# Kernel tuning notes

Hardware: AMD Instinct MI355X
Metric: run time of the kernel (lower is better)

Reference implementation:

```python
import jax, jax.numpy as jnp
import numpy as np

B, S_IN, T_OUT, H, L, V = 64, 512, 64, 1024, 2, 1024


def setup_inputs() -> dict:
    key = jax.random.key(0)
    ks = iter(jax.random.split(key, 64))
    def p(shape, scale=0.02):
        return (jax.random.normal(next(ks), shape, jnp.float32) * scale)
    d = {"x": jax.random.normal(next(ks), (B, 2, S_IN), jnp.float32)}
    d["emb"] = p((V, H))
    for l in range(L):
        i = 2 if l == 0 else H
        d[f"enc_Wih{l}"] = p((3 * H, i)); d[f"enc_Whh{l}"] = p((3 * H, H))
        d[f"enc_bih{l}"] = p((3 * H,));   d[f"enc_bhh{l}"] = p((3 * H,))
        d[f"dec_Wih{l}"] = p((H, H));     d[f"dec_Whh{l}"] = p((H, H))
        d[f"dec_bih{l}"] = p((H,));       d[f"dec_bhh{l}"] = p((H,))
    d["hq_W"] = p((H, H)); d["hq_b"] = p((H,))
    d["comb_W"] = p((H, 2 * H)); d["comb_b"] = p((H,))
    d["fc_W"] = p((V, H)); d["fc_b"] = p((V,))
    return d


def _gru_layer(x_seq, Wih, Whh, bih, bhh):
    # x_seq: [B,T,I] -> (outputs [B,T,H], h_T [B,H]). PyTorch GRU gate order r,z,n.
    xp = jnp.einsum('bti,gi->btg', x_seq, Wih) + bih  # [B,T,3H]
    h0 = jnp.zeros((x_seq.shape[0], Whh.shape[1]), x_seq.dtype)
    def step(h, xpt):
        hp = h @ Whh.T + bhh
        xr, xz, xn = jnp.split(xpt, 3, axis=-1)
        hr, hz, hn = jnp.split(hp, 3, axis=-1)
        r = jax.nn.sigmoid(xr + hr)
        z = jax.nn.sigmoid(xz + hz)
        n = jnp.tanh(xn + r * hn)
        h = (1.0 - z) * n + z * h
        return h, h
    hT, ys = jax.lax.scan(step, h0, jnp.swapaxes(xp, 0, 1))
    return jnp.swapaxes(ys, 0, 1), hT


def _forward(x, emb,
             enc_Wih0, enc_Whh0, enc_bih0, enc_bhh0,
             enc_Wih1, enc_Whh1, enc_bih1, enc_bhh1,
             dec_Wih0, dec_Whh0, dec_bih0, dec_bhh0,
             dec_Wih1, dec_Whh1, dec_bih1, dec_bhh1,
             hq_W, hq_b, comb_W, comb_b, fc_W, fc_b):
    enc_params = [(enc_Wih0, enc_Whh0, enc_bih0, enc_bhh0),
                  (enc_Wih1, enc_Whh1, enc_bih1, enc_bhh1)]
    dec_params = [(dec_Wih0, dec_Whh0, dec_bih0, dec_bhh0),
                  (dec_Wih1, dec_Whh1, dec_bih1, dec_bhh1)]
    # ---- encoder: GRU over x permuted to [B, S_in, 2] ----
    seq = jnp.transpose(x, (0, 2, 1)).astype(jnp.float32)
    h_enc = []
    for (Wih, Whh, bih, bhh) in enc_params:
        seq, hT = _gru_layer(seq, Wih, Whh, bih, bhh)
        h_enc.append(hT)
    enc_outs = seq                      # [B, S_in, H]
    hidden0 = jnp.stack(h_enc, axis=0)  # [L, B, H]

    tok0 = jnp.zeros((B,), jnp.int32)
    def dec_step(carry, _):
        tok, hid = carry
        inp = emb[tok]                  # [B, H]
        new_h = []
        for l, (Wih, Whh, bih, bhh) in enumerate(dec_params):
            h = jnp.tanh(inp @ Wih.T + bih + hid[l] @ Whh.T + bhh)
            new_h.append(h)
            inp = h
        hid = jnp.stack(new_h, axis=0)
        q = inp @ hq_W.T + hq_b                          # [B, H]
        scores = jnp.einsum('bsh,bh->bs', enc_outs, q)   # [B, S_in]
        aw = jax.nn.softmax(scores, axis=1)
        att = jnp.einsum('bs,bsh->bh', aw, enc_outs)     # [B, H]
        logits = jnp.concatenate([inp, att], axis=-1) @ comb_W.T + comb_b
        logits = logits @ fc_W.T + fc_b                  # [B, V]
        tok = jnp.argmax(logits, axis=-1).astype(jnp.int32)
        return (tok, hid), (logits, aw)
    (_, hidden), (logits_t, aw_t) = jax.lax.scan(dec_step, (tok0, hidden0), None, length=T_OUT)
    vec_out = jnp.swapaxes(logits_t, 0, 1)   # [B, T_out, V]
    attn = aw_t[-1][:, None, :]              # [B, 1, S_in] (last step, as in source)
    return vec_out, hidden, attn


def reference(x, emb,
              enc_Wih0, enc_Whh0, enc_bih0, enc_bhh0,
              enc_Wih1, enc_Whh1, enc_bih1, enc_bhh1,
              dec_Wih0, dec_Whh0, dec_bih0, dec_bhh0,
              dec_Wih1, dec_Whh1, dec_bih1, dec_bhh1,
              hq_W, hq_b, comb_W, comb_b, fc_W, fc_b):
    return _forward(x, emb,
                    enc_Wih0, enc_Whh0, enc_bih0, enc_bhh0,
                    enc_Wih1, enc_Whh1, enc_bih1, enc_bhh1,
                    dec_Wih0, dec_Whh0, dec_bih0, dec_bhh0,
                    dec_Wih1, dec_Whh1, dec_bih1, dec_bhh1,
                    hq_W, hq_b, comb_W, comb_b, fc_W, fc_b)
```

## Files before the change

### kernel.cpp

```cpp
#include <hip/hip_runtime.h>
#include <stdint.h>


#define BB 64
#define SS 512
#define TT 64
#define HH 1024
#define VV 1024
#define BH 65536
#define SH 524288
#define OFF_HID  4194304
#define OFF_ATTN 4325376

typedef _Float16 half8  __attribute__((ext_vector_type(8)));
typedef float    floatx4 __attribute__((ext_vector_type(4)));

struct P {
  const float *x, *emb;
  const float *eWih0, *eWhh0, *ebih0, *ebhh0;
  const float *dWih0, *dWhh0, *dbih0, *dbhh0;
  const float *eWih1, *eWhh1, *ebih1, *ebhh1;
  const float *dWih1, *dWhh1, *dbih1, *dbhh1;
  const float *hqW, *hqb, *combW, *combb, *fcW, *fcb;
  uint32_t* enc_i;
  _Float16 *W0h,*W0l;
  _Float16 *W1h,*W1l;
  _Float16 *embh,*embl,*T0h,*T0l;
  _Float16 *wih0dh,*wih0dl,*wih1dh,*wih1dl,*whh0dh,*whh0dl,*whh1dh,*whh1dl;
  _Float16 *hqh,*hql,*combh,*combl,*fch,*fcl;
  _Float16 *h0h,*h0l,*h1h,*h1l;
  _Float16 *dh0h,*dh0l,*dh1h,*dh1l;
  _Float16 *cath,*catl;
  _Float16 *ch,*cl;
  float *u0,*u1,*w1x,*q;
  float *attp_o;
  float *attp_ml;
  float *sc63;
  unsigned long long* amax;
  float* dout;
};

struct GSet { const _Float16 *Wh, *Wl, *Ah, *Al; const float *bias; float *out; };

__device__ __forceinline__ void splitf(float x, _Float16& hi, _Float16& lo){
  _Float16 h = (_Float16)x; hi = h;
  lo = (_Float16)((x - (float)h) * 2048.0f);
}
__device__ __forceinline__ float reconf(_Float16 hi, _Float16 lo){
  return fmaf((float)lo, 1.0f/2048.0f, (float)hi);
}
__device__ __forceinline__ float recon_u32(uint32_t w){
  float hi = (float)__builtin_bit_cast(_Float16, (unsigned short)(w & 0xffffu));
  float lo = (float)__builtin_bit_cast(_Float16, (unsigned short)(w >> 16));
  return fmaf(lo, 1.0f/2048.0f, hi);
}
__device__ __forceinline__ uint32_t pack_pair(float x){
  _Float16 hi, lo; splitf(x, hi, lo);
  return (uint32_t)__builtin_bit_cast(unsigned short, hi)
       | ((uint32_t)__builtin_bit_cast(unsigned short, lo) << 16);
}
__device__ __forceinline__ unsigned ordf(float f){
  unsigned u = __float_as_uint(f);
  return (u & 0x80000000u) ? ~u : (u | 0x80000000u);
}

template<int NT, int KH, bool SPLIT>
__device__ __forceinline__ void gemm_core(
    const _Float16* __restrict__ Ah0, const _Float16* __restrict__ Al0,
    const _Float16* __restrict__ Ah1, const _Float16* __restrict__ Al1,
    int sA,
    const _Float16* __restrict__ Wh, const _Float16* __restrict__ Wl,
    int nrows, _Float16* ldsW, float* accOut)
{
  const int tid = threadIdx.x, lane = tid & 63, wave = tid >> 6;
  const int mA = (wave<<4) + (lane & 15);
  const int kb = ((lane>>4) << 3);
  const int wstride = KH << 10;
  floatx4 aH[NT], aM1[NT], aM2[NT];
  int ne[NT];
  const _Float16* bh_base[NT];
  const _Float16* bl_base[NT];
  #pragma unroll
  for (int nt=0; nt<NT; ++nt){
    int nn = (lane & 15) + (nt<<4);
    ne[nt] = nn < nrows ? nn : nrows - 1;
    bh_base[nt] = ldsW + ne[nt]*1032 + kb;
    aH[nt]  = floatx4{0.f,0.f,0.f,0.f};
    aM1[nt] = floatx4{0.f,0.f,0.f,0.f};
    aM2[nt] = floatx4{0.f,0.f,0.f,0.f};
  }
  #pragma unroll
  for (int kh=0; kh<KH; ++kh){
    __syncthreads();
    const int iters = (nrows*128 + 255) >> 8;
    for (int it=0; it<iters; ++it){
      int idx = tid + (it<<8);
      int row = idx >> 7, col = (idx & 127) << 3;
      if (row < nrows)
        *(half8*)(ldsW + row*1032 + col) =
            *(const half8*)(Wh + row*wstride + (kh<<10) + col);
    }
    __syncthreads();
    const _Float16* ah_p = ((KH==2 && kh==1) ? Ah1 : Ah0) + mA*sA + kb;
    const _Float16* al_p = ((KH==2 && kh==1) ? Al1 : Al0) + mA*sA + kb;
    #pragma unroll
    for (int nt=0; nt<NT; ++nt) bl_base[nt] = Wl + ne[nt]*wstride + (kh<<10) + kb;
    #pragma unroll 4
    for (int ks=0; ks<32; ++ks){
      half8 ah = *(const half8*)(ah_p + (ks<<5));
      half8 al = *(const half8*)(al_p + (ks<<5));
      #pragma unroll
      for (int nt=0; nt<NT; ++nt){
        half8 bh = *(const half8*)(bh_base[nt] + (ks<<5));
        half8 bl = *(const half8*)(bl_base[nt] + (ks<<5));
        aH[nt]  = __builtin_amdgcn_mfma_f32_16x16x32_f16(ah, bh, aH[nt],  0,0,0);
        aM1[nt] = __builtin_amdgcn_mfma_f32_16x16x32_f16(ah, bl, aM1[nt], 0,0,0);
        aM2[nt] = __builtin_amdgcn_mfma_f32_16x16x32_f16(al, bh, aM2[nt], 0,0,0);
      }
    }
    if (SPLIT){
      #pragma unroll
      for (int nt=0; nt<NT; ++nt){
        #pragma unroll
        for (int r=0;r<4;++r)
          accOut[(kh*NT + nt)*4 + r] = aH[nt][r] + (aM1[nt][r] + aM2[nt][r]) * (1.f/2048.f);
        aH[nt]  = floatx4{0.f,0.f,0.f,0.f};
        aM1[nt] = floatx4{0.f,0.f,0.f,0.f};
        aM2[nt] = floatx4{0.f,0.f,0.f,0.f};
      }
    }
  }
  if (!SPLIT){
    #pragma unroll
    for (int nt=0; nt<NT; ++nt)
      #pragma unroll
      for (int r=0;r<4;++r)
        accOut[nt*4 + r] = aH[nt][r] + (aM1[nt][r] + aM2[nt][r]) * (1.f/2048.f);
  }
}

__global__ __launch_bounds__(256) void k_split(const float* __restrict__ src,
                                               _Float16* dh, _Float16* dl, int n){
  for (int i = blockIdx.x*256 + threadIdx.x; i < n; i += gridDim.x*256){
    _Float16 hi,lo; splitf(src[i],hi,lo); dh[i]=hi; dl[i]=lo;
  }
}

__global__ __launch_bounds__(256) void k_rw0(P p){
  const int n = 128*24*1024;
  for (int i = blockIdx.x*256 + threadIdx.x; i < n; i += gridDim.x*256){
    int k = i & 1023; int rest = i >> 10; int rr = rest % 24; int blk = rest / 24;
    int grow = (rr>>3)*1024 + (blk<<3) + (rr&7);
    _Float16 hi,lo; splitf(p.eWhh0[grow*1024 + k],hi,lo);
    p.W0h[i]=hi; p.W0l[i]=lo;
  }
}
__global__ __launch_bounds__(256) void k_rw1(P p){
  const int n = 128*24*2048;
  for (int i = blockIdx.x*256 + threadIdx.x; i < n; i += gridDim.x*256){
    int k = i & 2047; int rest = i >> 11; int rr = rest % 24; int blk = rest / 24;
    int grow = (rr>>3)*1024 + (blk<<3) + (rr&7);
    float v = (k < 1024) ? p.eWhh1[grow*1024 + k] : p.eWih1[grow*1024 + (k-1024)];
    _Float16 hi,lo; splitf(v,hi,lo);
    p.W1h[i]=hi; p.W1l[i]=lo;
  }
}
__global__ __launch_bounds__(256) void k_zero(P p){
  int i = blockIdx.x*256 + threadIdx.x;
  p.h1h[i] = (_Float16)0.f; p.h1l[i] = (_Float16)0.f;
  p.h0h[BH + i] = (_Float16)0.f; p.h0l[BH + i] = (_Float16)0.f;
}
__global__ __launch_bounds__(256) void k_t0(P p){
  __shared__ _Float16 ldsW[16*1032];
  const int ns = blockIdx.x & 63, mc = blockIdx.x >> 6;
  float acc[4];
  gemm_core<1,1,false>(p.embh + mc*65536, p.embl + mc*65536, nullptr, nullptr, 1024,
                       p.wih0dh + ns*16*1024, p.wih0dl + ns*16*1024, 16, ldsW, acc);
  const int lane = threadIdx.x & 63, wave = threadIdx.x >> 6;
  const int n = lane & 15, col = (ns<<4) + n;
  const float bv = p.dbih0[col];
  #pragma unroll
  for (int r=0;r<4;++r){
    int v = mc*64 + (wave<<4) + ((lane>>4)<<2) + r;
    _Float16 hi,lo; splitf(acc[r] + bv, hi, lo);
    p.T0h[v*1024 + col] = hi; p.T0l[v*1024 + col] = lo;
  }
}

__global__ __launch_bounds__(256) void k_enc(P p, int e){
  const int tid = threadIdx.x, lane = tid & 63, wave = tid >> 6;
  const bool is0 = blockIdx.x < 128;
  if (is0 && e >= 512) return;
  if (!is0 && e < 1) return;
  const int blk = is0 ? blockIdx.x : blockIdx.x - 128;
  const int j0 = blk << 3;

  __shared__ _Float16 ldsW[24*1032];
  __shared__ float ldsG[2][24][68];
  __shared__ float ldsC[24][4];

  if (tid < 24){
    int grow = (tid>>3)*1024 + j0 + (tid & 7);
    if (is0){
      ldsC[tid][0] = p.eWih0[grow*2+0];
      ldsC[tid][1] = p.eWih0[grow*2+1];
      ldsC[tid][2] = p.ebih0[grow];
      ldsC[tid][3] = p.ebhh0[grow];
    } else {
      ldsC[tid][0] = p.ebih1[grow];
      ldsC[tid][1] = p.ebhh1[grow];
    }
  }

  const int cur = e & 1, prv = cur ^ 1;
  float acc[16];
  if (is0){
    gemm_core<2,1,true>(p.h0h + prv*BH, p.h0l + prv*BH, nullptr, nullptr, 1024,
                        p.W0h + blk*24*1024, p.W0l + blk*24*1024, 24, ldsW, acc);
    #pragma unroll
    for (int nt=0; nt<2; ++nt){
      int n = (lane & 15) + (nt<<4);
      if (n < 24){
        #pragma unroll
        for (int r=0;r<4;++r)
          ldsG[0][n][(wave<<4)+((lane>>4)<<2)+r] = acc[nt*4+r];
      }
    }
  } else {
    gemm_core<2,2,true>(p.h1h + prv*BH, p.h1l + prv*BH,
                        p.h0h + prv*BH, p.h0l + prv*BH, 1024,
                        p.W1h + blk*24*2048, p.W1l + blk*24*2048, 24, ldsW, acc);
    #pragma unroll
    for (int kh=0; kh<2; ++kh){
      #pragma unroll
      for (int nt=0; nt<2; ++nt){
        int n = (lane & 15) + (nt<<4);
        if (n < 24){
          #pragma unroll
          for (int r=0;r<4;++r)
            ldsG[kh][n][(wave<<4)+((lane>>4)<<2)+r] = acc[(kh*2+nt)*4+r];
        }
      }
    }
  }
  __syncthreads();

  #pragma unroll
  for (int it=0; it<2; ++it){
    int idx = tid + (it<<8);
    int b = idx & 63, j = idx >> 6;
    int col = j0 + j;
    if (is0){
      int t = e;
      float hr = ldsG[0][j][b]    + ldsC[j][3];
      float hz = ldsG[0][8+j][b]  + ldsC[8+j][3];
      float hn = ldsG[0][16+j][b] + ldsC[16+j][3];
      float x0 = p.x[b*1024 + t], x1 = p.x[b*1024 + 512 + t];
      float xr = fmaf(x0, ldsC[j][0],    fmaf(x1, ldsC[j][1],    ldsC[j][2]));
      float xz = fmaf(x0, ldsC[8+j][0],  fmaf(x1, ldsC[8+j][1],  ldsC[8+j][2]));
      float xn = fmaf(x0, ldsC[16+j][0], fmaf(x1, ldsC[16+j][1], ldsC[16+j][2]));
      float rg = 1.0f/(1.0f + expf(-(xr+hr)));
      float zg = 1.0f/(1.0f + expf(-(xz+hz)));
      float ng = tanhf(xn + rg*hn);
      float hold = reconf(p.h0h[prv*BH + b*1024 + col], p.h0l[prv*BH + b*1024 + col]);
      float hnew = (1.0f - zg)*ng + zg*hold;
      _Float16 hi,lo; splitf(hnew,hi,lo);
      p.h0h[cur*BH + b*1024 + col] = hi;
      p.h0l[cur*BH + b*1024 + col] = lo;
    } else {
      int t = e - 1;
      float hr = ldsG[0][j][b]    + ldsC[j][1];
      float hz = ldsG[0][8+j][b]  + ldsC[8+j][1];
      float hn = ldsG[0][16+j][b] + ldsC[16+j][1];
      float xr = ldsG[1][j][b]    + ldsC[j][0];
      float xz = ldsG[1][8+j][b]  + ldsC[8+j][0];
      float xn = ldsG[1][16+j][b] + ldsC[16+j][0];
      float rg = 1.0f/(1.0f + expf(-(xr+hr)));
      float zg = 1.0f/(1.0f + expf(-(xz+hz)));
      float ng = tanhf(xn + rg*hn);
      float hold = reconf(p.h1h[prv*BH + b*1024 + col], p.h1l[prv*BH + b*1024 + col]);
      float hnew = (1.0f - zg)*ng + zg*hold;
      _Float16 hi,lo; splitf(hnew,hi,lo);
      p.h1h[cur*BH + b*1024 + col] = hi;
      p.h1l[cur*BH + b*1024 + col] = lo;
      p.enc_i[b*SH + t*1024 + col] = pack_pair(hnew);
    }
  }
}

__global__ __launch_bounds__(256) void k_dgemm2(GSet a, GSet b){
  const int tid = threadIdx.x, lane = tid & 63, wave = tid >> 6;
  const GSet g = blockIdx.x < 128 ? a : b;
  const int blk = blockIdx.x & 127;
  __shared__ _Float16 ldsW[8*1032];
  float acc[4];
  gemm_core<1,1,false>(g.Ah, g.Al, nullptr, nullptr, 1024,
                       g.Wh + blk*8*1024, g.Wl + blk*8*1024, 8, ldsW, acc);
  int n = lane & 15;
  if (n < 8){
    int col = (blk<<3) + n;
    float bv = g.bias[col];
    #pragma unroll
    for (int r=0;r<4;++r){
      int m = (wave<<4)+((lane>>4)<<2)+r;
      g.out[m*1024 + col] = acc[r] + bv;
    }
  }
}

__global__ __launch_bounds__(256) void k_dec0(P p, int t){
  const int tid = threadIdx.x, b = blockIdx.x;
  __shared__ unsigned long long red[256];
  unsigned long long v = 0;
  if (t > 0 && tid < 128) v = p.amax[b*128 + tid];
  red[tid] = v; __syncthreads();
  for (int off=128; off>=1; off>>=1){
    if (tid < off){ unsigned long long o = red[tid+off]; if (o > red[tid]) red[tid] = o; }
    __syncthreads();
  }
  const int tokb = (t > 0) ? (1023 - (int)(red[0] & 0xffffffffULL)) : 0;
  #pragma unroll
  for (int i=0;i<4;++i){
    int h = tid + (i<<8);
    float val = tanhf(reconf(p.T0h[tokb*1024+h], p.T0l[tokb*1024+h]) + p.u0[b*1024+h]);
    _Float16 hi,lo; splitf(val,hi,lo);
    p.dh0h[b*1024+h]=hi; p.dh0l[b*1024+h]=lo;
  }
}
__global__ __launch_bounds__(256) void k_dec2(P p){
  const int tid = threadIdx.x, b = blockIdx.x;
  #pragma unroll
  for (int i=0;i<4;++i){
    int h = tid + (i<<8);
    float val = tanhf(p.w1x[b*1024+h] + p.u1[b*1024+h]);
    _Float16 hi,lo; splitf(val,hi,lo);
    p.dh1h[b*1024+h]=hi; p.dh1l[b*1024+h]=lo;
    p.cath[b*2048+h]=hi; p.catl[b*2048+h]=lo;
  }
}
__global__ __launch_bounds__(256) void k_flash(P p, int t){
  const int tid = threadIdx.x, lane = tid & 63, wave = tid >> 6;
  const int b = blockIdx.x >> 1, half = blockIdx.x & 1;
  const int s0 = half << 8;
  const bool last = (t == 63);
  float qv[16];
  #pragma unroll
  for (int i=0;i<16;++i) qv[i] = p.q[b*1024 + (i<<6) + lane];
  float ov[16];
  #pragma unroll
  for (int i=0;i<16;++i) ov[i] = 0.f;
  float mrun = -3.0e38f, lrun = 0.f;
  for (int si=0; si<64; ++si){
    int s = s0 + (wave<<6) + si;
    const uint32_t* ep = p.enc_i + b*SH + s*1024 + lane;
    float ef[16]; float partial = 0.f;
    #pragma unroll
    for (int i=0;i<16;++i){
      ef[i] = recon_u32(ep[i<<6]);
      partial = fmaf(ef[i], qv[i], partial);
    }
    #pragma unroll
    for (int off=32; off; off>>=1) partial += __shfl_xor(partial, off, 64);
    if (last && lane == 0) p.sc63[b*512 + s] = partial;
    float mnew = fmaxf(mrun, partial);
    float fac = __expf(mrun - mnew);
    float w   = __expf(partial - mnew);
    lrun = fmaf(lrun, fac, w);
    #pragma unroll
    for (int i=0;i<16;++i) ov[i] = fmaf(ov[i], fac, w*ef[i]);
    mrun = mnew;
  }
  __shared__ float ldsO[4][1024];
  __shared__ float ldsM[4], ldsL2[4];
  #pragma unroll
  for (int i=0;i<16;++i) ldsO[wave][(i<<6)+lane] = ov[i];
  if (lane == 0){ ldsM[wave] = mrun; ldsL2[wave] = lrun; }
  __syncthreads();
  float M = fmaxf(fmaxf(ldsM[0],ldsM[1]), fmaxf(ldsM[2],ldsM[3]));
  float f0 = __expf(ldsM[0]-M), f1 = __expf(ldsM[1]-M),
        f2 = __expf(ldsM[2]-M), f3 = __expf(ldsM[3]-M);
  if (tid == 0){
    p.attp_ml[b*4 + half*2 + 0] = M;
    p.attp_ml[b*4 + half*2 + 1] = f0*ldsL2[0] + f1*ldsL2[1] + f2*ldsL2[2] + f3*ldsL2[3];
  }
  #pragma unroll
  for (int i=0;i<4;++i){
    int h = tid + (i<<8);
    p.attp_o[(b*2+half)*1024 + h] =
        f0*ldsO[0][h] + f1*ldsO[1][h] + f2*ldsO[2][h] + f3*ldsO[3][h];
  }
}
__global__ __launch_bounds__(256) void k_dec5(P p, int t){
  const int tid = threadIdx.x, b = blockIdx.x;
  float m0 = p.attp_ml[b*4+0], l0 = p.attp_ml[b*4+1];
  float m1 = p.attp_ml[b*4+2], l1 = p.attp_ml[b*4+3];
  float M = fmaxf(m0,m1);
  float f0 = expf(m0-M), f1 = expf(m1-M);
  float invL = 1.0f/(f0*l0 + f1*l1);
  #pragma unroll
  for (int i=0;i<4;++i){
    int h = tid + (i<<8);
    float o = (f0*p.attp_o[(b*2+0)*1024+h] + f1*p.attp_o[(b*2+1)*1024+h]) * invL;
    _Float16 hi,lo; splitf(o,hi,lo);
    p.cath[b*2048 + 1024 + h] = hi; p.catl[b*2048 + 1024 + h] = lo;
  }
  if (t == 63){
    #pragma unroll
    for (int i=0;i<2;++i){
      int s = tid + (i<<8);
      p.dout[OFF_ATTN + b*512 + s] = expf(p.sc63[b*512+s] - M) * invL;
    }
  }
}
__global__ __launch_bounds__(256) void k_comb(P p){
  const int tid = threadIdx.x, lane = tid & 63, wave = tid >> 6;
  const int blk = blockIdx.x;
  __shared__ _Float16 ldsW[8*1032];
  float acc[4];
  gemm_core<1,2,false>(p.cath, p.catl, p.cath + 1024, p.catl + 1024, 2048,
                       p.combh + blk*8*2048, p.combl + blk*8*2048, 8, ldsW, acc);
  int n = lane & 15;
  if (n < 8){
    int col = (blk<<3) + n;
    float bv = p.combb[col];
    #pragma unroll
    for (int r=0;r<4;++r){
      int m = (wave<<4)+((lane>>4)<<2)+r;
      _Float16 hi,lo; splitf(acc[r] + bv, hi, lo);
      p.ch[m*1024 + col] = hi; p.cl[m*1024 + col] = lo;
    }
  }
}
__global__ __launch_bounds__(256) void k_fc(P p, int t){
  const int tid = threadIdx.x, lane = tid & 63, wave = tid >> 6;
  const int blk = blockIdx.x;
  __shared__ _Float16 ldsW[8*1032];
  __shared__ float ldsL[8][68];
  float acc[4];
  gemm_core<1,1,false>(p.ch, p.cl, nullptr, nullptr, 1024,
                       p.fch + blk*8*1024, p.fcl + blk*8*1024, 8, ldsW, acc);
  int n = lane & 15;
  if (n < 8){
    int col = (blk<<3) + n;
    float bv = p.fcb[col];
    #pragma unroll
    for (int r=0;r<4;++r){
      int m = (wave<<4)+((lane>>4)<<2)+r;
      float val = acc[r] + bv;
      p.dout[m*65536 + t*1024 + col] = val;
      ldsL[n][m] = val;
    }
  }
  __syncthreads();
  if (tid < 64){
    int b = tid; float best = -3.0e38f; int bi = 0;
    #pragma unroll
    for (int jj=0; jj<8; ++jj){
      float v = ldsL[jj][b];
      if (v > best){ best = v; bi = jj; }
    }
    unsigned long long pk = ((unsigned long long)ordf(best) << 32)
                          | (unsigned)(1023 - ((blk<<3) + bi));
    p.amax[b*128 + blk] = pk;
  }
}
__global__ __launch_bounds__(256) void k_hidden(P p){
  int idx = blockIdx.x*256 + threadIdx.x;
  int i = idx & 65535;
  float v = (idx >> 16) ? reconf(p.dh1h[i], p.dh1l[i]) : reconf(p.dh0h[i], p.dh0l[i]);
  p.dout[OFF_HID + idx] = v;
}

extern "C" void kernel_launch(void* const* d_in, const int* in_sizes, int n_in,
                              void* d_out, int out_size, void* d_ws, size_t ws_size,
                              hipStream_t stream)
{
  (void)in_sizes; (void)n_in; (void)out_size;
  P p;
  p.x     = (const float*)d_in[0];  p.emb   = (const float*)d_in[1];
  p.eWih0 = (const float*)d_in[2];  p.eWhh0 = (const float*)d_in[3];
  p.ebih0 = (const float*)d_in[4];  p.ebhh0 = (const float*)d_in[5];
  p.dWih0 = (const float*)d_in[6];  p.dWhh0 = (const float*)d_in[7];
  p.dbih0 = (const float*)d_in[8];  p.dbhh0 = (const float*)d_in[9];
  p.eWih1 = (const float*)d_in[10]; p.eWhh1 = (const float*)d_in[11];
  p.ebih1 = (const float*)d_in[12]; p.ebhh1 = (const float*)d_in[13];
  p.dWih1 = (const float*)d_in[14]; p.dWhh1 = (const float*)d_in[15];
  p.dbih1 = (const float*)d_in[16]; p.dbhh1 = (const float*)d_in[17];
  p.hqW   = (const float*)d_in[18]; p.hqb   = (const float*)d_in[19];
  p.combW = (const float*)d_in[20]; p.combb = (const float*)d_in[21];
  p.fcW   = (const float*)d_in[22]; p.fcb   = (const float*)d_in[23];
  p.dout  = (float*)d_out;

  char* base = (char*)d_ws; size_t off = 0;
  auto alloc = [&](size_t bytes)->char*{
    char* r = base + off; off = (off + bytes + 255) & ~(size_t)255; return r;
  };
  p.enc_i = (uint32_t*)alloc(33554432ULL*4);
  p.W0h = (_Float16*)alloc(3145728ULL*2);  p.W0l = (_Float16*)alloc(3145728ULL*2);
  p.W1h = (_Float16*)alloc(6291456ULL*2);  p.W1l = (_Float16*)alloc(6291456ULL*2);
  p.embh = (_Float16*)alloc(1048576ULL*2); p.embl = (_Float16*)alloc(1048576ULL*2);
  p.T0h  = (_Float16*)alloc(1048576ULL*2); p.T0l  = (_Float16*)alloc(1048576ULL*2);
  p.wih0dh=(_Float16*)alloc(1048576ULL*2); p.wih0dl=(_Float16*)alloc(1048576ULL*2);
  p.wih1dh=(_Float16*)alloc(1048576ULL*2); p.wih1dl=(_Float16*)alloc(1048576ULL*2);
  p.whh0dh=(_Float16*)alloc(1048576ULL*2); p.whh0dl=(_Float16*)alloc(1048576ULL*2);
  p.whh1dh=(_Float16*)alloc(1048576ULL*2); p.whh1dl=(_Float16*)alloc(1048576ULL*2);
  p.hqh  = (_Float16*)alloc(1048576ULL*2); p.hql  = (_Float16*)alloc(1048576ULL*2);
  p.combh= (_Float16*)alloc(2097152ULL*2); p.combl= (_Float16*)alloc(2097152ULL*2);
  p.fch  = (_Float16*)alloc(1048576ULL*2); p.fcl  = (_Float16*)alloc(1048576ULL*2);
  p.h0h  = (_Float16*)alloc(131072ULL*2);  p.h0l  = (_Float16*)alloc(131072ULL*2);
  p.h1h  = (_Float16*)alloc(131072ULL*2);  p.h1l  = (_Float16*)alloc(131072ULL*2);
  p.dh0h = (_Float16*)alloc(65536ULL*2);   p.dh0l = (_Float16*)alloc(65536ULL*2);
  p.dh1h = (_Float16*)alloc(65536ULL*2);   p.dh1l = (_Float16*)alloc(65536ULL*2);
  p.cath = (_Float16*)alloc(131072ULL*2);  p.catl = (_Float16*)alloc(131072ULL*2);
  p.ch   = (_Float16*)alloc(65536ULL*2);   p.cl   = (_Float16*)alloc(65536ULL*2);
  p.u0   = (float*)alloc(65536ULL*4);      p.u1   = (float*)alloc(65536ULL*4);
  p.w1x  = (float*)alloc(65536ULL*4);      p.q    = (float*)alloc(65536ULL*4);
  p.attp_o  = (float*)alloc(131072ULL*4);
  p.attp_ml = (float*)alloc(256ULL*4);
  p.sc63    = (float*)alloc(32768ULL*4);
  p.amax    = (unsigned long long*)alloc(8192ULL*8);
  if (off > ws_size) return;

  k_split<<<2048,256,0,stream>>>(p.emb,   p.embh,   p.embl,   1048576);
  k_split<<<2048,256,0,stream>>>(p.dWih0, p.wih0dh, p.wih0dl, 1048576);
  k_split<<<2048,256,0,stream>>>(p.dWih1, p.wih1dh, p.wih1dl, 1048576);
  k_split<<<2048,256,0,stream>>>(p.dWhh0, p.whh0dh, p.whh0dl, 1048576);
  k_split<<<2048,256,0,stream>>>(p.dWhh1, p.whh1dh, p.whh1dl, 1048576);
  k_split<<<2048,256,0,stream>>>(p.hqW,   p.hqh,    p.hql,    1048576);
  k_split<<<2048,256,0,stream>>>(p.combW, p.combh,  p.combl,  2097152);
  k_split<<<2048,256,0,stream>>>(p.fcW,   p.fch,    p.fcl,    1048576);
  k_rw0<<<4096,256,0,stream>>>(p);
  k_rw1<<<4096,256,0,stream>>>(p);
  k_zero<<<256,256,0,stream>>>(p);
  k_t0<<<1024,256,0,stream>>>(p);

  for (int e=0; e<=512; ++e) k_enc<<<256,256,0,stream>>>(p, e);

  {
    GSet a{p.whh0dh, p.whh0dl, p.h0h + BH, p.h0l + BH, p.dbhh0, p.u0};
    GSet b{p.whh1dh, p.whh1dl, p.h1h,      p.h1l,      p.dbhh1, p.u1};
    k_dgemm2<<<256,256,0,stream>>>(a, b);
  }
  GSet sK1a{p.wih1dh, p.wih1dl, p.dh0h, p.dh0l, p.dbih1, p.w1x};
  GSet sK1b{p.whh0dh, p.whh0dl, p.dh0h, p.dh0l, p.dbhh0, p.u0};
  GSet sK3a{p.hqh,    p.hql,    p.dh1h, p.dh1l, p.hqb,   p.q};
  GSet sK3b{p.whh1dh, p.whh1dl, p.dh1h, p.dh1l, p.dbhh1, p.u1};

  for (int t=0; t<64; ++t){
    k_dec0<<<64,256,0,stream>>>(p, t);
    k_dgemm2<<<256,256,0,stream>>>(sK1a, sK1b);
    k_dec2<<<64,256,0,stream>>>(p);
    k_dgemm2<<<256,256,0,stream>>>(sK3a, sK3b);
    k_flash<<<128,256,0,stream>>>(p, t);
    k_dec5<<<64,256,0,stream>>>(p, t);
    k_comb<<<128,256,0,stream>>>(p);
    k_fc<<<128,256,0,stream>>>(p, t);
  }
  k_hidden<<<512,256,0,stream>>>(p);
}
```

Measured before the change: 30.33 ms.

## Fuse encoder timestep launches into one persistent cooperative kernel with grid barrier

Replaces the 513 per-timestep encoder kernel launches with a single cooperative persistent kernel that loops over time and synchronizes all 256 blocks through an atomic grid barrier. Each block loads its slice of the recurrent weights into LDS once (about 112KB dynamic shared memory) instead of reloading them every step, removing launch overhead and repeated weight traffic. The risks are spin-barrier latency, the large LDS footprint forcing one block per CU, and the layer-1 low half of the weights still being read from global memory each step. If the cooperative launch fails, it falls back to the old per-step launches.

```diff
diff --git a/kernel.cpp b/kernel.cpp
--- a/kernel.cpp
+++ b/kernel.cpp
@@ -37,6 +37,7 @@
   float *attp_ml;
   float *sc63;
   unsigned long long* amax;
+  unsigned* bar;
   float* dout;
 };
 
@@ -62,6 +63,17 @@
 __device__ __forceinline__ unsigned ordf(float f){
   unsigned u = __float_as_uint(f);
   return (u & 0x80000000u) ? ~u : (u | 0x80000000u);
+}
+
+__device__ __forceinline__ void gbar(unsigned* bar, unsigned target){
+  __syncthreads();
+  if (threadIdx.x == 0){
+    __threadfence();
+    atomicAdd(bar, 1u);
+    while (atomicAdd(bar, 0u) < target) __builtin_amdgcn_s_sleep(1);
+    __threadfence();
+  }
+  __syncthreads();
 }
 
 template<int NT, int KH, bool SPLIT>
@@ -169,6 +181,7 @@
   int i = blockIdx.x*256 + threadIdx.x;
   p.h1h[i] = (_Float16)0.f; p.h1l[i] = (_Float16)0.f;
   p.h0h[BH + i] = (_Float16)0.f; p.h0l[BH + i] = (_Float16)0.f;
+  if (blockIdx.x == 0 && threadIdx.x == 0) *p.bar = 0u;
 }
 __global__ __launch_bounds__(256) void k_t0(P p){
   __shared__ _Float16 ldsW[16*1032];
@@ -184,6 +197,183 @@
     int v = mc*64 + (wave<<4) + ((lane>>4)<<2) + r;
     _Float16 hi,lo; splitf(acc[r] + bv, hi, lo);
     p.T0h[v*1024 + col] = hi; p.T0l[v*1024 + col] = lo;
+  }
+}
+
+__global__ __launch_bounds__(256) void k_encp(P p){
+  extern __shared__ __align__(16) char smem[];
+  const int tid = threadIdx.x, lane = tid & 63, wave = tid >> 6;
+  const bool is0 = blockIdx.x < 128;
+  const int blk = is0 ? (int)blockIdx.x : (int)blockIdx.x - 128;
+  const int j0 = blk << 3;
+
+  _Float16* Wh = (_Float16*)smem;
+  _Float16* Wl = Wh + 24*1032;
+  float* ldsGf = (float*)(smem + 99072);
+  float* ldsCf = ldsGf + 2*24*68;
+
+  if (is0){
+    const _Float16* gh = p.W0h + blk*24*1024;
+    const _Float16* gl = p.W0l + blk*24*1024;
+    for (int it = tid; it < 24*128; it += 256){
+      int row = it >> 7, col = (it & 127) << 3;
+      *(half8*)(Wh + row*1032 + col) = *(const half8*)(gh + row*1024 + col);
+      *(half8*)(Wl + row*1032 + col) = *(const half8*)(gl + row*1024 + col);
+    }
+  } else {
+    const _Float16* gh = p.W1h + blk*24*2048;
+    for (int it = tid; it < 24*256; it += 256){
+      int row = it >> 8, col = (it & 255) << 3;
+      *(half8*)(Wh + row*2056 + col) = *(const half8*)(gh + row*2048 + col);
+    }
+  }
+  if (tid < 24){
+    int grow = (tid>>3)*1024 + j0 + (tid & 7);
+    if (is0){
+      ldsCf[tid*4+0] = p.eWih0[grow*2+0];
+      ldsCf[tid*4+1] = p.eWih0[grow*2+1];
+      ldsCf[tid*4+2] = p.ebih0[grow];
+      ldsCf[tid*4+3] = p.ebhh0[grow];
+    } else {
+      ldsCf[tid*4+0] = p.ebih1[grow];
+      ldsCf[tid*4+1] = p.ebhh1[grow];
+    }
+  }
+  __syncthreads();
+
+  const int mA = (wave<<4) + (lane & 15);
+  const int kb = ((lane>>4) << 3);
+  int ne[2];
+  #pragma unroll
+  for (int nt=0; nt<2; ++nt){
+    int nn = (lane & 15) + (nt<<4);
+    ne[nt] = nn < 24 ? nn : 23;
+  }
+
+  for (int e = 0; e <= 512; ++e){
+    const int cur = e & 1, prv = cur ^ 1;
+    if (is0){
+      if (e < 512){
+        floatx4 aH[2], aM1[2], aM2[2];
+        #pragma unroll
+        for (int nt=0; nt<2; ++nt){
+          aH[nt]=floatx4{0.f,0.f,0.f,0.f};
+          aM1[nt]=floatx4{0.f,0.f,0.f,0.f};
+          aM2[nt]=floatx4{0.f,0.f,0.f,0.f};
+        }
+        const _Float16* ah_p = p.h0h + prv*BH + mA*1024 + kb;
+        const _Float16* al_p = p.h0l + prv*BH + mA*1024 + kb;
+        #pragma unroll 4
+        for (int ks=0; ks<32; ++ks){
+          half8 ah = *(const half8*)(ah_p + (ks<<5));
+          half8 al = *(const half8*)(al_p + (ks<<5));
+          #pragma unroll
+          for (int nt=0; nt<2; ++nt){
+            half8 bh = *(const half8*)(Wh + ne[nt]*1032 + kb + (ks<<5));
+            half8 bl = *(const half8*)(Wl + ne[nt]*1032 + kb + (ks<<5));
+            aH[nt]  = __builtin_amdgcn_mfma_f32_16x16x32_f16(ah, bh, aH[nt],  0,0,0);
+            aM1[nt] = __builtin_amdgcn_mfma_f32_16x16x32_f16(ah, bl, aM1[nt], 0,0,0);
+            aM2[nt] = __builtin_amdgcn_mfma_f32_16x16x32_f16(al, bh, aM2[nt], 0,0,0);
+          }
+        }
+        #pragma unroll
+        for (int nt=0; nt<2; ++nt){
+          int n = (lane & 15) + (nt<<4);
+          if (n < 24){
+            #pragma unroll
+            for (int r=0;r<4;++r)
+              ldsGf[n*68 + (wave<<4)+((lane>>4)<<2)+r] =
+                  aH[nt][r] + (aM1[nt][r] + aM2[nt][r]) * (1.f/2048.f);
+          }
+        }
+        __syncthreads();
+        #pragma unroll
+        for (int it=0; it<2; ++it){
+          int idx = tid + (it<<8);
+          int b = idx & 63, j = idx >> 6;
+          int col = j0 + j;
+          float hr = ldsGf[j*68+b]      + ldsCf[j*4+3];
+          float hz = ldsGf[(8+j)*68+b]  + ldsCf[(8+j)*4+3];
+          float hn = ldsGf[(16+j)*68+b] + ldsCf[(16+j)*4+3];
+          float x0 = p.x[b*1024 + e], x1 = p.x[b*1024 + 512 + e];
+          float xr = fmaf(x0, ldsCf[j*4+0],      fmaf(x1, ldsCf[j*4+1],      ldsCf[j*4+2]));
+          float xz = fmaf(x0, ldsCf[(8+j)*4+0],  fmaf(x1, ldsCf[(8+j)*4+1],  ldsCf[(8+j)*4+2]));
+          float xn = fmaf(x0, ldsCf[(16+j)*4+0], fmaf(x1, ldsCf[(16+j)*4+1], ldsCf[(16+j)*4+2]));
+          float rg = 1.0f/(1.0f + expf(-(xr+hr)));
+          float zg = 1.0f/(1.0f + expf(-(xz+hz)));
+          float ng = tanhf(xn + rg*hn);
+          float hold = reconf(p.h0h[prv*BH + b*1024 + col], p.h0l[prv*BH + b*1024 + col]);
+          float hnew = (1.0f - zg)*ng + zg*hold;
+          _Float16 hi,lo; splitf(hnew,hi,lo);
+          p.h0h[cur*BH + b*1024 + col] = hi;
+          p.h0l[cur*BH + b*1024 + col] = lo;
+        }
+      }
+    } else {
+      if (e >= 1){
+        #pragma unroll
+        for (int kh=0; kh<2; ++kh){
+          floatx4 aH[2], aM1[2], aM2[2];
+          #pragma unroll
+          for (int nt=0; nt<2; ++nt){
+            aH[nt]=floatx4{0.f,0.f,0.f,0.f};
+            aM1[nt]=floatx4{0.f,0.f,0.f,0.f};
+            aM2[nt]=floatx4{0.f,0.f,0.f,0.f};
+          }
+          const _Float16* ah_p = (kh ? p.h0h : p.h1h) + prv*BH + mA*1024 + kb;
+          const _Float16* al_p = (kh ? p.h0l : p.h1l) + prv*BH + mA*1024 + kb;
+          const _Float16* wlb  = p.W1l + blk*24*2048 + (kh<<10) + kb;
+          const _Float16* whb  = Wh + (kh<<10) + kb;
+          #pragma unroll 4
+          for (int ks=0; ks<32; ++ks){
+            half8 ah = *(const half8*)(ah_p + (ks<<5));
+            half8 al = *(const half8*)(al_p + (ks<<5));
+            #pragma unroll
+            for (int nt=0; nt<2; ++nt){
+              half8 bh = *(const half8*)(whb + ne[nt]*2056 + (ks<<5));
+              half8 bl = *(const half8*)(wlb + ne[nt]*2048 + (ks<<5));
+              aH[nt]  = __builtin_amdgcn_mfma_f32_16x16x32_f16(ah, bh, aH[nt],  0,0,0);
+              aM1[nt] = __builtin_amdgcn_mfma_f32_16x16x32_f16(ah, bl, aM1[nt], 0,0,0);
+              aM2[nt] = __builtin_amdgcn_mfma_f32_16x16x32_f16(al, bh, aM2[nt], 0,0,0);
+            }
+          }
+          #pragma unroll
+          for (int nt=0; nt<2; ++nt){
+            int n = (lane & 15) + (nt<<4);
+            if (n < 24){
+              #pragma unroll
+              for (int r=0;r<4;++r)
+                ldsGf[(kh*24+n)*68 + (wave<<4)+((lane>>4)<<2)+r] =
+                    aH[nt][r] + (aM1[nt][r] + aM2[nt][r]) * (1.f/2048.f);
+            }
+          }
+        }
+        __syncthreads();
+        #pragma unroll
+        for (int it=0; it<2; ++it){
+          int idx = tid + (it<<8);
+          int b = idx & 63, j = idx >> 6;
+          int col = j0 + j;
+          int t = e - 1;
+          float hr = ldsGf[j*68+b]         + ldsCf[j*4+1];
+          float hz = ldsGf[(8+j)*68+b]     + ldsCf[(8+j)*4+1];
+          float hn = ldsGf[(16+j)*68+b]    + ldsCf[(16+j)*4+1];
+          float xr = ldsGf[(24+j)*68+b]    + ldsCf[j*4+0];
+          float xz = ldsGf[(24+8+j)*68+b]  + ldsCf[(8+j)*4+0];
+          float xn = ldsGf[(24+16+j)*68+b] + ldsCf[(16+j)*4+0];
+          float rg = 1.0f/(1.0f + expf(-(xr+hr)));
+          float zg = 1.0f/(1.0f + expf(-(xz+hz)));
+          float ng = tanhf(xn + rg*hn);
+          float hold = reconf(p.h1h[prv*BH + b*1024 + col], p.h1l[prv*BH + b*1024 + col]);
+          float hnew = (1.0f - zg)*ng + zg*hold;
+          _Float16 hi,lo; splitf(hnew,hi,lo);
+          p.h1h[cur*BH + b*1024 + col] = hi;
+          p.h1l[cur*BH + b*1024 + col] = lo;
+          p.enc_i[b*SH + t*1024 + col] = pack_pair(hnew);
+        }
+      }
+    }
+    gbar(p.bar, (unsigned)(e+1)*256u);
   }
 }
 
@@ -519,6 +709,7 @@
   p.attp_ml = (float*)alloc(256ULL*4);
   p.sc63    = (float*)alloc(32768ULL*4);
   p.amax    = (unsigned long long*)alloc(8192ULL*8);
+  p.bar     = (unsigned*)alloc(256);
   if (off > ws_size) return;
 
   k_split<<<2048,256,0,stream>>>(p.emb,   p.embh,   p.embl,   1048576);
@@ -534,7 +725,15 @@
   k_zero<<<256,256,0,stream>>>(p);
   k_t0<<<1024,256,0,stream>>>(p);
 
-  for (int e=0; e<=512; ++e) k_enc<<<256,256,0,stream>>>(p, e);
+  {
+    void* kargs[] = { (void*)&p };
+    hipError_t ce = hipLaunchCooperativeKernel(
+        reinterpret_cast<const void*>(&k_encp), dim3(256), dim3(256),
+        kargs, 112512u, stream);
+    if (ce != hipSuccess){
+      for (int e=0; e<=512; ++e) k_enc<<<256,256,0,stream>>>(p, e);
+    }
+  }
 
   {
     GSet a{p.whh0dh, p.whh0dl, p.h0h + BH, p.h0l + BH, p.dbhh0, p.u0};
```

Result: slower. 38.71 ms (+27.6%).

## Run encoder recurrence as one persistent kernel with grid barriers

Applied to the files above, without the earlier changes.

Replaces the 513 per-timestep encoder launches with a single persistent kernel of 512 blocks that keeps each block's weight slice resident in LDS and synchronizes timesteps through an atomic grid barrier. Each block now owns 4 hidden columns (12 gate rows) instead of 8, and the previous hidden value is carried in a register instead of being reloaded. This removes per-step launch overhead and the repeated weight reload from global memory. The cost is reliance on all 512 blocks being co-resident at two blocks per CU. If the barrier spin bound is hit, the kernel aborts, and the per-step fallback only runs when the launch itself reports an error, not on a barrier timeout.

```diff
diff --git a/kernel.cpp b/kernel.cpp
--- a/kernel.cpp
+++ b/kernel.cpp
@@ -37,6 +37,7 @@
   float *attp_ml;
   float *sc63;
   unsigned long long* amax;
+  unsigned* bar;
   float* dout;
 };
 
@@ -62,6 +63,34 @@
 __device__ __forceinline__ unsigned ordf(float f){
   unsigned u = __float_as_uint(f);
   return (u & 0x80000000u) ? ~u : (u | 0x80000000u);
+}
+
+__device__ __forceinline__ int gbar(unsigned* bar, unsigned target, int bound){
+  __shared__ int oks;
+  __syncthreads();
+  if (threadIdx.x == 0){
+    int ok = 1;
+    __threadfence();
+    __hip_atomic_fetch_add(bar, 1u, __ATOMIC_RELAXED, __HIP_MEMORY_SCOPE_AGENT);
+    int it = 0;
+    for (;;){
+      unsigned v = ((it & 63) == 63)
+        ? __hip_atomic_fetch_add(bar, 0u, __ATOMIC_RELAXED, __HIP_MEMORY_SCOPE_AGENT)
+        : __hip_atomic_load(bar, __ATOMIC_RELAXED, __HIP_MEMORY_SCOPE_AGENT);
+      if (v >= 0x40000000u){ ok = 0; break; }
+      if (v >= target) break;
+      ++it;
+      if (bound && it > bound){
+        __hip_atomic_fetch_add(bar, 0x40000000u, __ATOMIC_RELAXED, __HIP_MEMORY_SCOPE_AGENT);
+        ok = 0; break;
+      }
+      __builtin_amdgcn_s_sleep(8);
+    }
+    __threadfence();
+    oks = ok;
+  }
+  __syncthreads();
+  return oks;
 }
 
 template<int NT, int KH, bool SPLIT>
@@ -147,19 +176,19 @@
 }
 
 __global__ __launch_bounds__(256) void k_rw0(P p){
-  const int n = 128*24*1024;
+  const int n = 256*12*1024;
   for (int i = blockIdx.x*256 + threadIdx.x; i < n; i += gridDim.x*256){
-    int k = i & 1023; int rest = i >> 10; int rr = rest % 24; int blk = rest / 24;
-    int grow = (rr>>3)*1024 + (blk<<3) + (rr&7);
+    int k = i & 1023; int rest = i >> 10; int rr = rest % 12; int blk = rest / 12;
+    int grow = (rr>>2)*1024 + (blk<<2) + (rr&3);
     _Float16 hi,lo; splitf(p.eWhh0[grow*1024 + k],hi,lo);
     p.W0h[i]=hi; p.W0l[i]=lo;
   }
 }
 __global__ __launch_bounds__(256) void k_rw1(P p){
-  const int n = 128*24*2048;
+  const int n = 256*12*2048;
   for (int i = blockIdx.x*256 + threadIdx.x; i < n; i += gridDim.x*256){
-    int k = i & 2047; int rest = i >> 11; int rr = rest % 24; int blk = rest / 24;
-    int grow = (rr>>3)*1024 + (blk<<3) + (rr&7);
+    int k = i & 2047; int rest = i >> 11; int rr = rest % 12; int blk = rest / 12;
+    int grow = (rr>>2)*1024 + (blk<<2) + (rr&3);
     float v = (k < 1024) ? p.eWhh1[grow*1024 + k] : p.eWih1[grow*1024 + (k-1024)];
     _Float16 hi,lo; splitf(v,hi,lo);
     p.W1h[i]=hi; p.W1l[i]=lo;
@@ -169,6 +198,7 @@
   int i = blockIdx.x*256 + threadIdx.x;
   p.h1h[i] = (_Float16)0.f; p.h1l[i] = (_Float16)0.f;
   p.h0h[BH + i] = (_Float16)0.f; p.h0l[BH + i] = (_Float16)0.f;
+  if (blockIdx.x == 0 && threadIdx.x == 0) *p.bar = 0u;
 }
 __global__ __launch_bounds__(256) void k_t0(P p){
   __shared__ _Float16 ldsW[16*1032];
@@ -187,78 +217,232 @@
   }
 }
 
-__global__ __launch_bounds__(256) void k_enc(P p, int e){
+__global__ __launch_bounds__(256,2) void k_encp(P p){
+  __shared__ _Float16 ldsW[24768];
+  __shared__ float ldsG[2*12*68];
+  __shared__ float ldsC[12*4];
   const int tid = threadIdx.x, lane = tid & 63, wave = tid >> 6;
-  const bool is0 = blockIdx.x < 128;
+  const bool is0 = blockIdx.x < 256;
+  const int blk = is0 ? (int)blockIdx.x : (int)blockIdx.x - 256;
+  const int j0 = blk << 2;
+
+  if (is0){
+    const _Float16* gh = p.W0h + blk*12*1024;
+    const _Float16* gl = p.W0l + blk*12*1024;
+    _Float16* Wl = ldsW + 12*1032;
+    for (int it = tid; it < 12*128; it += 256){
+      int row = it >> 7, col = (it & 127) << 3;
+      *(half8*)(ldsW + row*1032 + col) = *(const half8*)(gh + row*1024 + col);
+      *(half8*)(Wl   + row*1032 + col) = *(const half8*)(gl + row*1024 + col);
+    }
+  } else {
+    const _Float16* gh = p.W1h + blk*12*2048;
+    for (int it = tid; it < 12*256; it += 256){
+      int row = it >> 8, col = (it & 255) << 3;
+      *(half8*)(ldsW + row*2056 + col) = *(const half8*)(gh + row*2048 + col);
+    }
+  }
+  if (tid < 12){
+    int grow = (tid>>2)*1024 + j0 + (tid & 3);
+    if (is0){
+      ldsC[tid*4+0] = p.eWih0[grow*2+0];
+      ldsC[tid*4+1] = p.eWih0[grow*2+1];
+      ldsC[tid*4+2] = p.ebih0[grow];
+      ldsC[tid*4+3] = p.ebhh0[grow];
+    } else {
+      ldsC[tid*4+0] = p.ebih1[grow];
+      ldsC[tid*4+1] = p.ebhh1[grow];
+    }
+  }
+
+  if (!gbar(p.bar, 512u, 2000000)) return;
+
+  const int mA = (wave<<4) + (lane & 15);
+  const int kb = ((lane>>4) << 3);
+  const int nn = lane & 15;
+  const int ne = nn < 12 ? nn : 11;
+  const int b_ep = tid & 63, c_ep = tid >> 6;
+  const int col_ep = j0 + c_ep;
+  float hold = 0.f;
+
+  for (int e = 0; e <= 512; ++e){
+    const int cur = e & 1, prv = cur ^ 1;
+    if (is0){
+      if (e < 512){
+        floatx4 aH{0.f,0.f,0.f,0.f}, aM1{0.f,0.f,0.f,0.f}, aM2{0.f,0.f,0.f,0.f};
+        const _Float16* ah_p = p.h0h + prv*BH + mA*1024 + kb;
+        const _Float16* al_p = p.h0l + prv*BH + mA*1024 + kb;
+        const _Float16* bh_p = ldsW + ne*1032 + kb;
+        const _Float16* bl_p = ldsW + 12*1032 + ne*1032 + kb;
+        #pragma unroll 4
+        for (int ks=0; ks<32; ++ks){
+          half8 ah = *(const half8*)(ah_p + (ks<<5));
+          half8 al = *(const half8*)(al_p + (ks<<5));
+          half8 bh = *(const half8*)(bh_p + (ks<<5));
+          half8 bl = *(const half8*)(bl_p + (ks<<5));
+          aH  = __builtin_amdgcn_mfma_f32_16x16x32_f16(ah, bh, aH,  0,0,0);
+          aM1 = __builtin_amdgcn_mfma_f32_16x16x32_f16(ah, bl, aM1, 0,0,0);
+          aM2 = __builtin_amdgcn_mfma_f32_16x16x32_f16(al, bh, aM2, 0,0,0);
+        }
+        if (nn < 12){
+          #pragma unroll
+          for (int r=0;r<4;++r)
+            ldsG[nn*68 + (wave<<4)+((lane>>4)<<2)+r] =
+                aH[r] + (aM1[r] + aM2[r]) * (1.f/2048.f);
+        }
+        __syncthreads();
+        {
+          const int b = b_ep, c = c_ep, col = col_ep;
+          float hr = ldsG[c*68+b]     + ldsC[c*4+3];
+          float hz = ldsG[(4+c)*68+b] + ldsC[(4+c)*4+3];
+          float hn = ldsG[(8+c)*68+b] + ldsC[(8+c)*4+3];
+          float x0 = p.x[b*1024 + e], x1 = p.x[b*1024 + 512 + e];
+          float xr = fmaf(x0, ldsC[c*4+0],     fmaf(x1, ldsC[c*4+1],     ldsC[c*4+2]));
+          float xz = fmaf(x0, ldsC[(4+c)*4+0], fmaf(x1, ldsC[(4+c)*4+1], ldsC[(4+c)*4+2]));
+          float xn = fmaf(x0, ldsC[(8+c)*4+0], fmaf(x1, ldsC[(8+c)*4+1], ldsC[(8+c)*4+2]));
+          float rg = 1.0f/(1.0f + expf(-(xr+hr)));
+          float zg = 1.0f/(1.0f + expf(-(xz+hz)));
+          float ng = tanhf(xn + rg*hn);
+          float hnew = (1.0f - zg)*ng + zg*hold;
+          _Float16 hi,lo; splitf(hnew,hi,lo);
+          hold = reconf(hi,lo);
+          p.h0h[cur*BH + b*1024 + col] = hi;
+          p.h0l[cur*BH + b*1024 + col] = lo;
+        }
+      }
+    } else {
+      if (e >= 1){
+        #pragma unroll
+        for (int kh=0; kh<2; ++kh){
+          floatx4 aH{0.f,0.f,0.f,0.f}, aM1{0.f,0.f,0.f,0.f}, aM2{0.f,0.f,0.f,0.f};
+          const _Float16* ah_p = (kh ? p.h0h : p.h1h) + prv*BH + mA*1024 + kb;
+          const _Float16* al_p = (kh ? p.h0l : p.h1l) + prv*BH + mA*1024 + kb;
+          const _Float16* bh_p = ldsW + ne*2056 + (kh<<10) + kb;
+          const _Float16* bl_p = p.W1l + blk*12*2048 + ne*2048 + (kh<<10) + kb;
+          #pragma unroll 4
+          for (int ks=0; ks<32; ++ks){
+            half8 ah = *(const half8*)(ah_p + (ks<<5));
+            half8 al = *(const half8*)(al_p + (ks<<5));
+            half8 bh = *(const half8*)(bh_p + (ks<<5));
+            half8 bl = *(const half8*)(bl_p + (ks<<5));
+            aH  = __builtin_amdgcn_mfma_f32_16x16x32_f16(ah, bh, aH,  0,0,0);
+            aM1 = __builtin_amdgcn_mfma_f32_16x16x32_f16(ah, bl, aM1, 0,0,0);
+            aM2 = __builtin_amdgcn_mfma_f32_16x16x32_f16(al, bh, aM2, 0,0,0);
+          }
+          if (nn < 12){
+            #pragma unroll
+            for (int r=0;r<4;++r)
+              ldsG[(kh*12+nn)*68 + (wave<<4)+((lane>>4)<<2)+r] =
+                  aH[r] + (aM1[r] + aM2[r]) * (1.f/2048.f);
+          }
+        }
+        __syncthreads();
+        {
+          const int b = b_ep, c = c_ep, col = col_ep;
+          const int t = e - 1;
+          float hr = ldsG[c*68+b]        + ldsC[c*4+1];
+          float hz = ldsG[(4+c)*68+b]    + ldsC[(4+c)*4+1];
+          float hn = ldsG[(8+c)*68+b]    + ldsC[(8+c)*4+1];
+          float xr = ldsG[(12+c)*68+b]   + ldsC[c*4+0];
+          float xz = ldsG[(12+4+c)*68+b] + ldsC[(4+c)*4+0];
+          float xn = ldsG[(12+8+c)*68+b] + ldsC[(8+c)*4+0];
+          float rg = 1.0f/(1.0f + expf(-(xr+hr)));
+          float zg = 1.0f/(1.0f + expf(-(xz+hz)));
+          float ng = tanhf(xn + rg*hn);
+          float hnew = (1.0f - zg)*ng + zg*hold;
+          _Float16 hi,lo; splitf(hnew,hi,lo);
+          hold = reconf(hi,lo);
+          p.h1h[cur*BH + b*1024 + col] = hi;
+          p.h1l[cur*BH + b*1024 + col] = lo;
+          p.enc_i[b*SH + t*1024 + col] = pack_pair(hnew);
+        }
+      }
+    }
+    if (!gbar(p.bar, (unsigned)(e+2)*512u, 100000)) return;
+  }
+}
+
+__global__ __launch_bounds__(256,2) void k_enc(P p, int e){
+  __shared__ _Float16 ldsW[24768];
+  __shared__ float ldsG[2*12*68];
+  __shared__ float ldsC[12*4];
+  const int tid = threadIdx.x, lane = tid & 63, wave = tid >> 6;
+  const bool is0 = blockIdx.x < 256;
   if (is0 && e >= 512) return;
   if (!is0 && e < 1) return;
-  const int blk = is0 ? blockIdx.x : blockIdx.x - 128;
-  const int j0 = blk << 3;
-
-  __shared__ _Float16 ldsW[24*1032];
-  __shared__ float ldsG[2][24][68];
-  __shared__ float ldsC[24][4];
-
-  if (tid < 24){
-    int grow = (tid>>3)*1024 + j0 + (tid & 7);
+  const int blk = is0 ? (int)blockIdx.x : (int)blockIdx.x - 256;
+  const int j0 = blk << 2;
+
+  if (is0){
+    const _Float16* gh = p.W0h + blk*12*1024;
+    const _Float16* gl = p.W0l + blk*12*1024;
+    _Float16* Wl = ldsW + 12*1032;
+    for (int it = tid; it < 12*128; it += 256){
+      int row = it >> 7, col = (it & 127) << 3;
+      *(half8*)(ldsW + row*1032 + col) = *(const half8*)(gh + row*1024 + col);
+      *(half8*)(Wl   + row*1032 + col) = *(const half8*)(gl + row*1024 + col);
+    }
+  } else {
+    const _Float16* gh = p.W1h + blk*12*2048;
+    for (int it = tid; it < 12*256; it += 256){
+      int row = it >> 8, col = (it & 255) << 3;
+      *(half8*)(ldsW + row*2056 + col) = *(const half8*)(gh + row*2048 + col);
+    }
+  }
+  if (tid < 12){
+    int grow = (tid>>2)*1024 + j0 + (tid & 3);
     if (is0){
-      ldsC[tid][0] = p.eWih0[grow*2+0];
-      ldsC[tid][1] = p.eWih0[grow*2+1];
-      ldsC[tid][2] = p.ebih0[grow];
-      ldsC[tid][3] = p.ebhh0[grow];
+      ldsC[tid*4+0] = p.eWih0[grow*2+0];
+      ldsC[tid*4+1] = p.eWih0[grow*2+1];
+      ldsC[tid*4+2] = p.ebih0[grow];
+      ldsC[tid*4+3] = p.ebhh0[grow];
     } else {
-      ldsC[tid][0] = p.ebih1[grow];
-      ldsC[tid][1] = p.ebhh1[grow];
-    }
-  }
+      ldsC[tid*4+0] = p.ebih1[grow];
+      ldsC[tid*4+1] = p.ebhh1[grow];
+    }
+  }
+  __syncthreads();
 
   const int cur = e & 1, prv = cur ^ 1;
-  float acc[16];
+  const int mA = (wave<<4) + (lane & 15);
+  const int kb = ((lane>>4) << 3);
+  const int nn = lane & 15;
+  const int ne = nn < 12 ? nn : 11;
+  const int b_ep = tid & 63, c_ep = tid >> 6;
+  const int col_ep = j0 + c_ep;
+
   if (is0){
-    gemm_core<2,1,true>(p.h0h + prv*BH, p.h0l + prv*BH, nullptr, nullptr, 1024,
-                        p.W0h + blk*24*1024, p.W0l + blk*24*1024, 24, ldsW, acc);
-    #pragma unroll
-    for (int nt=0; nt<2; ++nt){
-      int n = (lane & 15) + (nt<<4);
-      if (n < 24){
-        #pragma unroll
-        for (int r=0;r<4;++r)
-          ldsG[0][n][(wave<<4)+((lane>>4)<<2)+r] = acc[nt*4+r];
-      }
-    }
-  } else {
-    gemm_core<2,2,true>(p.h1h + prv*BH, p.h1l + prv*BH,
-                        p.h0h + prv*BH, p.h0l + prv*BH, 1024,
-                        p.W1h + blk*24*2048, p.W1l + blk*24*2048, 24, ldsW, acc);
-    #pragma unroll
-    for (int kh=0; kh<2; ++kh){
+    floatx4 aH{0.f,0.f,0.f,0.f}, aM1{0.f,0.f,0.f,0.f}, aM2{0.f,0.f,0.f,0.f};
+    const _Float16* ah_p = p.h0h + prv*BH + mA*1024 + kb;
+    const _Float16* al_p = p.h0l + prv*BH + mA*1024 + kb;
+    const _Float16* bh_p = ldsW + ne*1032 + kb;
+    const _Float16* bl_p = ldsW + 12*1032 + ne*1032 + kb;
+    #pragma unroll 4
+    for (int ks=0; ks<32; ++ks){
+      half8 ah = *(const half8*)(ah_p + (ks<<5));
+      half8 al = *(const half8*)(al_p + (ks<<5));
+      half8 bh = *(const half8*)(bh_p + (ks<<5));
+      half8 bl = *(const half8*)(bl_p + (ks<<5));
+      aH  = __builtin_amdgcn_mfma_f32_16x16x32_f16(ah, bh, aH,  0,0,0);
+      aM1 = __builtin_amdgcn_mfma_f32_16x16x32_f16(ah, bl, aM1, 0,0,0);
+      aM2 = __builtin_amdgcn_mfma_f32_16x16x32_f16(al, bh, aM2, 0,0,0);
+    }
+    if (nn < 12){
       #pragma unroll
-      for (int nt=0; nt<2; ++nt){
-        int n = (lane & 15) + (nt<<4);
-        if (n < 24){
-          #pragma unroll
-          for (int r=0;r<4;++r)
-            ldsG[kh][n][(wave<<4)+((lane>>4)<<2)+r] = acc[(kh*2+nt)*4+r];
-        }
-      }
-    }
-  }
-  __syncthreads();
-
-  #pragma unroll
-  for (int it=0; it<2; ++it){
-    int idx = tid + (it<<8);
-    int b = idx & 63, j = idx >> 6;
-    int col = j0 + j;
-    if (is0){
-      int t = e;
-      float hr = ldsG[0][j][b]    + ldsC[j][3];
-      float hz = ldsG[0][8+j][b]  + ldsC[8+j][3];
-      float hn = ldsG[0][16+j][b] + ldsC[16+j][3];
-      float x0 = p.x[b*1024 + t], x1 = p.x[b*1024 + 512 + t];
-      float xr = fmaf(x0, ldsC[j][0],    fmaf(x1, ldsC[j][1],    ldsC[j][2]));
-      float xz = fmaf(x0, ldsC[8+j][0],  fmaf(x1, ldsC[8+j][1],  ldsC[8+j][2]));
-      float xn = fmaf(x0, ldsC[16+j][0], fmaf(x1, ldsC[16+j][1], ldsC[16+j][2]));
+      for (int r=0;r<4;++r)
+        ldsG[nn*68 + (wave<<4)+((lane>>4)<<2)+r] =
+            aH[r] + (aM1[r] + aM2[r]) * (1.f/2048.f);
+    }
+    __syncthreads();
+    {
+      const int b = b_ep, c = c_ep, col = col_ep;
+      float hr = ldsG[c*68+b]     + ldsC[c*4+3];
+      float hz = ldsG[(4+c)*68+b] + ldsC[(4+c)*4+3];
+      float hn = ldsG[(8+c)*68+b] + ldsC[(8+c)*4+3];
+      float x0 = p.x[b*1024 + e], x1 = p.x[b*1024 + 512 + e];
+      float xr = fmaf(x0, ldsC[c*4+0],     fmaf(x1, ldsC[c*4+1],     ldsC[c*4+2]));
+      float xz = fmaf(x0, ldsC[(4+c)*4+0], fmaf(x1, ldsC[(4+c)*4+1], ldsC[(4+c)*4+2]));
+      float xn = fmaf(x0, ldsC[(8+c)*4+0], fmaf(x1, ldsC[(8+c)*4+1], ldsC[(8+c)*4+2]));
       float rg = 1.0f/(1.0f + expf(-(xr+hr)));
       float zg = 1.0f/(1.0f + expf(-(xz+hz)));
       float ng = tanhf(xn + rg*hn);
@@ -267,14 +451,42 @@
       _Float16 hi,lo; splitf(hnew,hi,lo);
       p.h0h[cur*BH + b*1024 + col] = hi;
       p.h0l[cur*BH + b*1024 + col] = lo;
-    } else {
-      int t = e - 1;
-      float hr = ldsG[0][j][b]    + ldsC[j][1];
-      float hz = ldsG[0][8+j][b]  + ldsC[8+j][1];
-      float hn = ldsG[0][16+j][b] + ldsC[16+j][1];
-      float xr = ldsG[1][j][b]    + ldsC[j][0];
-      float xz = ldsG[1][8+j][b]  + ldsC[8+j][0];
-      float xn = ldsG[1][16+j][b] + ldsC[16+j][0];
+    }
+  } else {
+    #pragma unroll
+    for (int kh=0; kh<2; ++kh){
+      floatx4 aH{0.f,0.f,0.f,0.f}, aM1{0.f,0.f,0.f,0.f}, aM2{0.f,0.f,0.f,0.f};
+      const _Float16* ah_p = (kh ? p.h0h : p.h1h) + prv*BH + mA*1024 + kb;
+      const _Float16* al_p = (kh ? p.h0l : p.h1l) + prv*BH + mA*1024 + kb;
+      const _Float16* bh_p = ldsW + ne*2056 + (kh<<10) + kb;
+      const _Float16* bl_p = p.W1l + blk*12*2048 + ne*2048 + (kh<<10) + kb;
+      #pragma unroll 4
+      for (int ks=0; ks<32; ++ks){
+        half8 ah = *(const half8*)(ah_p + (ks<<5));
+        half8 al = *(const half8*)(al_p + (ks<<5));
+        half8 bh = *(const half8*)(bh_p + (ks<<5));
+        half8 bl = *(const half8*)(bl_p + (ks<<5));
+        aH  = __builtin_amdgcn_mfma_f32_16x16x32_f16(ah, bh, aH,  0,0,0);
+        aM1 = __builtin_amdgcn_mfma_f32_16x16x32_f16(ah, bl, aM1, 0,0,0);
+        aM2 = __builtin_amdgcn_mfma_f32_16x16x32_f16(al, bh, aM2, 0,0,0);
+      }
+      if (nn < 12){
+        #pragma unroll
+        for (int r=0;r<4;++r)
+          ldsG[(kh*12+nn)*68 + (wave<<4)+((lane>>4)<<2)+r] =
+              aH[r] + (aM1[r] + aM2[r]) * (1.f/2048.f);
+      }
+    }
+    __syncthreads();
+    {
+      const int b = b_ep, c = c_ep, col = col_ep;
+      const int t = e - 1;
+      float hr = ldsG[c*68+b]        + ldsC[c*4+1];
+      float hz = ldsG[(4+c)*68+b]    + ldsC[(4+c)*4+1];
+      float hn = ldsG[(8+c)*68+b]    + ldsC[(8+c)*4+1];
+      float xr = ldsG[(12+c)*68+b]   + ldsC[c*4+0];
+      float xz = ldsG[(12+4+c)*68+b] + ldsC[(4+c)*4+0];
+      float xn = ldsG[(12+8+c)*68+b] + ldsC[(8+c)*4+0];
       float rg = 1.0f/(1.0f + expf(-(xr+hr)));
       float zg = 1.0f/(1.0f + expf(-(xz+hz)));
       float ng = tanhf(xn + rg*hn);
@@ -519,6 +731,7 @@
   p.attp_ml = (float*)alloc(256ULL*4);
   p.sc63    = (float*)alloc(32768ULL*4);
   p.amax    = (unsigned long long*)alloc(8192ULL*8);
+  p.bar     = (unsigned*)alloc(256);
   if (off > ws_size) return;
 
   k_split<<<2048,256,0,stream>>>(p.emb,   p.embh,   p.embl,   1048576);
@@ -534,7 +747,11 @@
   k_zero<<<256,256,0,stream>>>(p);
   k_t0<<<1024,256,0,stream>>>(p);
 
-  for (int e=0; e<=512; ++e) k_enc<<<256,256,0,stream>>>(p, e);
+  (void)hipGetLastError();
+  k_encp<<<512,256,0,stream>>>(p);
+  if (hipGetLastError() != hipSuccess){
+    for (int e=0; e<=512; ++e) k_enc<<<512,256,0,stream>>>(p, e);
+  }
 
   {
     GSet a{p.whh0dh, p.whh0dl, p.h0h + BH, p.h0l + BH, p.dbhh0, p.u0};
```

Measured after the change: 55.73 ms. 83.8% more time.
